# Optimization experiments

Hardware: AMD Instinct MI355X
Metric: run time of the kernel (lower is better)

## Reference

```python
import jax, jax.numpy as jnp
import numpy as np

N_NODES = 100000
N_EDGES = 1600000
D_IN = 128
D_HID = 128
N_CLS = 2


def gcn_conv(x, edge_index, W, b):
    """PyG GCNConv: add self-loops, symmetric normalization, linear, scatter-add, bias."""
    n = x.shape[0]
    loop = jnp.arange(n, dtype=edge_index.dtype)
    src = jnp.concatenate([edge_index[0], loop])  # [E+N]
    dst = jnp.concatenate([edge_index[1], loop])
    # degree computed on destination (col) after adding self-loops
    deg = jax.ops.segment_sum(jnp.ones_like(dst, dtype=x.dtype), dst, num_segments=n)
    dinv = jnp.where(deg > 0, jax.lax.rsqrt(deg), 0.0)
    norm = dinv[src] * dinv[dst]  # [E+N]
    h = x @ W  # [N, out]
    msg = h[src] * norm[:, None]  # [E+N, out]
    out = jax.ops.segment_sum(msg, dst, num_segments=n)
    return out + b


def setup_inputs() -> dict:
    key = jax.random.key(0)
    k1, k2, k3, k4 = jax.random.split(key, 4)
    x = jax.random.normal(k1, (N_NODES, D_IN), dtype=jnp.float32)
    edge_index = jax.random.randint(k2, (2, N_EDGES), 0, N_NODES, dtype=jnp.int64)
    W1 = jax.random.normal(k3, (D_IN, D_HID), dtype=jnp.float32) * (1.0 / np.sqrt(D_IN))
    b1 = jnp.zeros((D_HID,), dtype=jnp.float32)
    W2 = jax.random.normal(k4, (D_HID, N_CLS), dtype=jnp.float32) * (1.0 / np.sqrt(D_HID))
    b2 = jnp.zeros((N_CLS,), dtype=jnp.float32)
    return {"x": x, "edge_index": edge_index, "W1": W1, "b1": b1, "W2": W2, "b2": b2}


def reference(x, edge_index, W1, b1, W2, b2):
    h = gcn_conv(x, edge_index, W1, b1)
    h = jax.nn.relu(h)
    # training=False -> dropout skipped
    out = gcn_conv(h, edge_index, W2, b2)
    return out
```

## Files before the change

### kernel.cpp

```cpp
#include <hip/hip_runtime.h>
#include <hip/hip_fp16.h>
#include <cstdint>
#include <cstddef>

#define NN 100000
#define NE 1600000
#define D 128
#define NBK 782
#define NBLK_P 200
#define EPB 8000
#define CAP 3072

typedef _Float16 half8 __attribute__((ext_vector_type(8)));
typedef _Float16 half4v __attribute__((ext_vector_type(4)));
typedef float f32x4 __attribute__((ext_vector_type(4)));


__launch_bounds__(256)
__global__ void pscat_k(const int* __restrict__ ei, unsigned* __restrict__ gcnt,
                        unsigned* __restrict__ part,
                        const float* __restrict__ W, _Float16* __restrict__ Wt) {
    __shared__ unsigned hist[NBK];
    __shared__ unsigned run[NBK];
    int tid = threadIdx.x, b = blockIdx.x;
    for (int k = tid; k < NBK; k += 256) hist[k] = 0u;
    __syncthreads();
    int e0 = b * EPB;
    for (int i = tid * 4; i < EPB; i += 1024) {
        int4 d4 = *(const int4*)(ei + NE + e0 + i);
        atomicAdd(&hist[d4.x >> 7], 1u);
        atomicAdd(&hist[d4.y >> 7], 1u);
        atomicAdd(&hist[d4.z >> 7], 1u);
        atomicAdd(&hist[d4.w >> 7], 1u);
    }
    __syncthreads();
    for (int k = tid; k < NBK; k += 256) {
        unsigned c = hist[k];
        run[k] = c ? atomicAdd(&gcnt[k * 16], c) : 0u;
    }
    if (b < 64) {
        int idx = b * 256 + tid;
        int n = idx >> 7, kk = idx & 127;
        Wt[idx] = (_Float16)W[kk * 128 + n];
    }
    __syncthreads();
    for (int i = tid * 4; i < EPB; i += 1024) {
        int4 s4 = *(const int4*)(ei + e0 + i);
        int4 d4 = *(const int4*)(ei + NE + e0 + i);
        unsigned k, slot;
        k = (unsigned)(d4.x >> 7); slot = atomicAdd(&run[k], 1u);
        if (slot < CAP) part[(size_t)k * CAP + slot] = (unsigned)s4.x | ((unsigned)(d4.x & 127) << 20);
        k = (unsigned)(d4.y >> 7); slot = atomicAdd(&run[k], 1u);
        if (slot < CAP) part[(size_t)k * CAP + slot] = (unsigned)s4.y | ((unsigned)(d4.y & 127) << 20);
        k = (unsigned)(d4.z >> 7); slot = atomicAdd(&run[k], 1u);
        if (slot < CAP) part[(size_t)k * CAP + slot] = (unsigned)s4.z | ((unsigned)(d4.z & 127) << 20);
        k = (unsigned)(d4.w >> 7); slot = atomicAdd(&run[k], 1u);
        if (slot < CAP) part[(size_t)k * CAP + slot] = (unsigned)s4.w | ((unsigned)(d4.w & 127) << 20);
    }
}

__launch_bounds__(256)
__global__ void p4_csr_k(const unsigned* __restrict__ part, const unsigned* __restrict__ gcnt,
                         unsigned* __restrict__ rp, unsigned* __restrict__ re,
                         float* __restrict__ dinv, unsigned* __restrict__ col) {
    __shared__ unsigned c[128], p[128], run[128];
    int tid = threadIdx.x, k = blockIdx.x;
    int n0 = k << 7;
    int nodes = (NN - n0 < 128) ? (NN - n0) : 128;
    unsigned cnt = gcnt[k * 16];
    if (cnt > CAP) cnt = CAP;
    unsigned e0c = (unsigned)k * CAP;
    const unsigned* pk = part + (size_t)k * CAP;

    if (tid < 128) c[tid] = 0u;
    __syncthreads();
    for (unsigned t = tid; t < cnt; t += 256)
        atomicAdd(&c[(pk[t] >> 20) & 127], 1u);
    __syncthreads();

    unsigned myc = (tid < 128) ? c[tid] : 0u;
    if (tid < 128) p[tid] = myc;
    __syncthreads();
    for (int off = 1; off < 128; off <<= 1) {
        unsigned u = 0;
        if (tid < 128 && tid >= off) u = p[tid - off];
        __syncthreads();
        if (tid < 128) p[tid] += u;
        __syncthreads();
    }
    if (tid < 128) {
        unsigned excl = p[tid] - myc;
        run[tid] = excl;
        if (tid < nodes) {
            rp[n0 + tid] = e0c + excl;
            re[n0 + tid] = e0c + excl + myc;
            dinv[n0 + tid] = rsqrtf((float)(myc + 1u));
        }
    }
    __syncthreads();

    for (unsigned t = tid; t < cnt; t += 256) {
        unsigned v = pk[t];
        unsigned dlo = (v >> 20) & 127;
        unsigned pos = e0c + atomicAdd(&run[dlo], 1u);
        col[pos] = v & 0xFFFFFu;
    }
}

__launch_bounds__(256)
__global__ void gemm1_k(const float* __restrict__ x, const _Float16* __restrict__ Wt,
                        const float* __restrict__ dinv, _Float16* __restrict__ h) {
    __shared__ _Float16 wt[128 * 136];
    __shared__ _Float16 xs[128 * 72];
    int tid = threadIdx.x;
    int rb = blockIdx.x * 128;
    int w = tid >> 6, lane = tid & 63;
    int m = lane & 15, q4 = lane >> 4;

#pragma unroll
    for (int q = 0; q < 8; q++) {
        int idx = q * 256 + tid;
        int n = idx >> 4, k8 = (idx & 15) * 8;
        *(half8*)(&wt[n * 136 + k8]) = *(const half8*)(Wt + n * 128 + k8);
    }

    f32x4 acc[2][8];
#pragma unroll
    for (int rt = 0; rt < 2; rt++)
#pragma unroll
        for (int nt = 0; nt < 8; nt++) acc[rt][nt] = (f32x4){0.f, 0.f, 0.f, 0.f};

    for (int ks = 0; ks <= 64; ks += 64) {
        if (ks) __syncthreads();
#pragma unroll
        for (int q = 0; q < 8; q++) {
            int idx = q * 256 + tid;
            int row = idx >> 4;
            int c4 = (idx & 15) * 4;
            int gr = rb + row;
            float4 v = (gr < NN) ? *(const float4*)(x + (size_t)gr * 128 + ks + c4)
                                 : make_float4(0, 0, 0, 0);
            half4v hv = { (_Float16)v.x, (_Float16)v.y, (_Float16)v.z, (_Float16)v.w };
            *(half4v*)(&xs[row * 72 + c4]) = hv;
        }
        __syncthreads();

#pragma unroll
        for (int kc = 0; kc < 2; kc++) {
            half8 a0 = *(const half8*)(&xs[(w * 32 + m) * 72 + kc * 32 + q4 * 8]);
            half8 a1 = *(const half8*)(&xs[(w * 32 + 16 + m) * 72 + kc * 32 + q4 * 8]);
#pragma unroll
            for (int nt = 0; nt < 8; nt++) {
                half8 bf = *(const half8*)(&wt[(nt * 16 + m) * 136 + ks + kc * 32 + q4 * 8]);
                acc[0][nt] = __builtin_amdgcn_mfma_f32_16x16x32_f16(a0, bf, acc[0][nt], 0, 0, 0);
                acc[1][nt] = __builtin_amdgcn_mfma_f32_16x16x32_f16(a1, bf, acc[1][nt], 0, 0, 0);
            }
        }
    }

    float dv[2][4];
#pragma unroll
    for (int rt = 0; rt < 2; rt++)
#pragma unroll
        for (int r = 0; r < 4; r++) {
            int ri = rb + w * 32 + rt * 16 + q4 * 4 + r;
            dv[rt][r] = (ri < NN) ? dinv[ri] : 0.f;
        }
    __syncthreads();
#pragma unroll
    for (int rt = 0; rt < 2; rt++)
#pragma unroll
        for (int nt = 0; nt < 8; nt++)
#pragma unroll
            for (int r = 0; r < 4; r++)
                wt[(w * 32 + rt * 16 + q4 * 4 + r) * 136 + nt * 16 + m] =
                    (_Float16)(acc[rt][nt][r] * dv[rt][r]);
    __syncthreads();
#pragma unroll
    for (int q = 0; q < 8; q++) {
        int idx = q * 256 + tid;
        int row = idx >> 4;
        int c8 = (idx & 15) * 8;
        int gr = rb + row;
        if (gr < NN)
            *(half8*)(h + (size_t)gr * 128 + c8) = *(const half8*)(&wt[row * 136 + c8]);
    }
}

__launch_bounds__(256)
__global__ void agg1_k(const _Float16* __restrict__ h, const unsigned* __restrict__ rp,
                       const unsigned* __restrict__ re, const unsigned* __restrict__ col,
                       const float* __restrict__ dinv, const float* __restrict__ b1,
                       const float* __restrict__ W2, float* __restrict__ z) {
    int i = (blockIdx.x * 256 + threadIdx.x) >> 6;
    int lane = threadIdx.x & 63;
    if (i >= NN) return;
    unsigned si = __builtin_amdgcn_readfirstlane((unsigned)i);

    const __half2* hb = (const __half2*)h;
    unsigned p0 = __builtin_amdgcn_readfirstlane(rp[si]);
    unsigned p1 = __builtin_amdgcn_readfirstlane(re[si]);
    int deg = (int)(p1 - p0);

    unsigned cv = col[p0 + (unsigned)lane];

    int degc = deg > 64 ? 64 : deg;
    int R = (degc + 15) >> 4;
    float2 sv = __half22float2(hb[(size_t)si * 64u + lane]);
    float f = (float)(1 + degc - 16 * R);
    float ax = f * sv.x, ay = f * sv.y;

#define ROUND16(r)                                                           \
    {                                                                        \
        float2 vv[16];                                                       \
        _Pragma("unroll")                                                    \
        for (int t = 0; t < 16; t++) {                                       \
            int k = (r) * 16 + t;                                            \
            unsigned s = (k < degc) ? __builtin_amdgcn_readlane(cv, k) : si; \
            vv[t] = __half22float2(hb[(size_t)s * 64u + lane]);              \
        }                                                                    \
        ax += ((vv[0].x + vv[1].x) + (vv[2].x + vv[3].x))                    \
            + ((vv[4].x + vv[5].x) + (vv[6].x + vv[7].x))                    \
            + ((vv[8].x + vv[9].x) + (vv[10].x + vv[11].x))                  \
            + ((vv[12].x + vv[13].x) + (vv[14].x + vv[15].x));               \
        ay += ((vv[0].y + vv[1].y) + (vv[2].y + vv[3].y))                    \
            + ((vv[4].y + vv[5].y) + (vv[6].y + vv[7].y))                    \
            + ((vv[8].y + vv[9].y) + (vv[10].y + vv[11].y))                  \
            + ((vv[12].y + vv[13].y) + (vv[14].y + vv[15].y));               \
    }

    if (degc > 0)  ROUND16(0)
    if (degc > 16) ROUND16(1)
    if (degc > 32) ROUND16(2)
    if (degc > 48) ROUND16(3)
#undef ROUND16

    for (unsigned e = p0 + 64; e < p1; ++e) {
        unsigned s_ = __builtin_amdgcn_readfirstlane(col[e]);
        float2 v = __half22float2(hb[(size_t)s_ * 64u + lane]);
        ax += v.x;
        ay += v.y;
    }

    float di = dinv[si];
    ax *= di;
    ay *= di;

    float2 bv = ((const float2*)b1)[lane];
    float h0 = fmaxf(ax + bv.x, 0.f);
    float h1 = fmaxf(ay + bv.y, 0.f);

    float4 w = ((const float4*)W2)[lane];
    float pz0 = fmaf(h0, w.x, h1 * w.z);
    float pz1 = fmaf(h0, w.y, h1 * w.w);
#pragma unroll
    for (int off = 32; off > 0; off >>= 1) {
        pz0 += __shfl_down(pz0, off);
        pz1 += __shfl_down(pz1, off);
    }
    if (lane == 0) {
        float2* zp = (float2*)(z + (size_t)si * 2);
        *zp = make_float2(pz0 * di, pz1 * di);
    }
}

__launch_bounds__(256)
__global__ void agg2_k(const float* __restrict__ z, const unsigned* __restrict__ rp,
                       const unsigned* __restrict__ re, const unsigned* __restrict__ col,
                       const float* __restrict__ dinv, const float* __restrict__ b2,
                       float* __restrict__ out) {
    int i = (blockIdx.x * 256 + threadIdx.x) >> 4;
    int sl = threadIdx.x & 15;
    if (i >= NN) return;

    unsigned p0 = rp[i], p1 = re[i];
    float a0 = 0.f, a1 = 0.f;
    for (unsigned e = p0 + sl; e < p1; e += 16) {
        unsigned s = col[e];
        float2 v = ((const float2*)z)[s];
        a0 += v.x;
        a1 += v.y;
    }
#pragma unroll
    for (int off = 8; off > 0; off >>= 1) {
        a0 += __shfl_down(a0, off, 16);
        a1 += __shfl_down(a1, off, 16);
    }
    if (sl == 0) {
        float di = dinv[i];
        float2 zi = ((const float2*)z)[i];
        out[(size_t)i * 2]     = (a0 + zi.x) * di + b2[0];
        out[(size_t)i * 2 + 1] = (a1 + zi.y) * di + b2[1];
    }
}

extern "C" void kernel_launch(void* const* d_in, const int* in_sizes, int n_in,
                              void* d_out, int out_size, void* d_ws, size_t ws_size,
                              hipStream_t stream) {
    const float* x  = (const float*)d_in[0];
    const int*   ei = (const int*)d_in[1];
    const float* W1 = (const float*)d_in[2];
    const float* b1 = (const float*)d_in[3];
    const float* W2 = (const float*)d_in[4];
    const float* b2 = (const float*)d_in[5];
    float* out = (float*)d_out;

    char* ws = (char*)d_ws;
    unsigned* part = (unsigned*)(ws);
    unsigned* gcnt = (unsigned*)(ws + 9609216);
    _Float16* h    = (_Float16*)(ws);
    float*    z    = (float*)(ws + 25600000);
    float*    dinv = (float*)(ws + 26400000);
    unsigned* rp   = (unsigned*)(ws + 26800000);
    unsigned* re   = (unsigned*)(ws + 27200000);
    unsigned* col  = (unsigned*)(ws + 27600000);
    _Float16* Wt   = (_Float16*)(ws + 37300000);

    hipMemsetAsync(gcnt, 0, 782 * 16 * sizeof(unsigned), stream);
    pscat_k<<<NBLK_P, 256, 0, stream>>>(ei, gcnt, part, W1, Wt);
    p4_csr_k<<<NBK, 256, 0, stream>>>(part, gcnt, rp, re, dinv, col);

    gemm1_k<<<(NN + 127) / 128, 256, 0, stream>>>(x, Wt, dinv, h);
    agg1_k<<<(NN * 64 + 255) / 256, 256, 0, stream>>>(h, rp, re, col, dinv, b1, W2, z);
    agg2_k<<<(NN * 16 + 255) / 256, 256, 0, stream>>>(z, rp, re, col, dinv, b2, out);
}
```

Measured before the change: 221.1 us.

## Fuse CSR build kernel with first-layer GEMM into one kernel

Merges the per-bucket CSR construction kernel and the X·W1 MFMA GEMM into a single kernel, since both use 128-node blocks. The degree-based dinv is kept in shared memory and reused for row scaling, so it is not reloaded from global memory, and one kernel launch is removed. The h buffer moves to a separate workspace region because it previously aliased the partition buffer that the fused kernel still reads. The cost is a larger per-block shared-memory footprint, and the GEMM can no longer overlap independently with the CSR work.

After: 219.6 us. About the same (-0.7%).

```diff
diff --git a/kernel.cpp b/kernel.cpp
--- a/kernel.cpp
+++ b/kernel.cpp
@@ -60,41 +60,60 @@
 }
 
 __launch_bounds__(256)
-__global__ void p4_csr_k(const unsigned* __restrict__ part, const unsigned* __restrict__ gcnt,
-                         unsigned* __restrict__ rp, unsigned* __restrict__ re,
-                         float* __restrict__ dinv, unsigned* __restrict__ col) {
-    __shared__ unsigned c[128], p[128], run[128];
+__global__ void p4g_k(const unsigned* __restrict__ part, const unsigned* __restrict__ gcnt,
+                      const float* __restrict__ x, const _Float16* __restrict__ Wt,
+                      unsigned* __restrict__ rp, unsigned* __restrict__ re,
+                      float* __restrict__ dinv, unsigned* __restrict__ col,
+                      _Float16* __restrict__ h) {
+    __shared__ __align__(16) _Float16 wt[128 * 136];
+    __shared__ __align__(16) _Float16 xs[128 * 72];
+    __shared__ float dinvs[128];
+    unsigned* cc  = (unsigned*)xs;
+    unsigned* pp  = cc + 128;
+    unsigned* run = pp + 128;
     int tid = threadIdx.x, k = blockIdx.x;
     int n0 = k << 7;
     int nodes = (NN - n0 < 128) ? (NN - n0) : 128;
+    int w = tid >> 6, lane = tid & 63;
+    int m = lane & 15, q4 = lane >> 4;
+
+#pragma unroll
+    for (int q = 0; q < 8; q++) {
+        int idx = q * 256 + tid;
+        int n = idx >> 4, k8 = (idx & 15) * 8;
+        *(half8*)(&wt[n * 136 + k8]) = *(const half8*)(Wt + n * 128 + k8);
+    }
+
     unsigned cnt = gcnt[k * 16];
     if (cnt > CAP) cnt = CAP;
     unsigned e0c = (unsigned)k * CAP;
     const unsigned* pk = part + (size_t)k * CAP;
 
-    if (tid < 128) c[tid] = 0u;
+    if (tid < 128) cc[tid] = 0u;
     __syncthreads();
     for (unsigned t = tid; t < cnt; t += 256)
-        atomicAdd(&c[(pk[t] >> 20) & 127], 1u);
-    __syncthreads();
-
-    unsigned myc = (tid < 128) ? c[tid] : 0u;
-    if (tid < 128) p[tid] = myc;
+        atomicAdd(&cc[(pk[t] >> 20) & 127], 1u);
+    __syncthreads();
+
+    unsigned myc = (tid < 128) ? cc[tid] : 0u;
+    if (tid < 128) pp[tid] = myc;
     __syncthreads();
     for (int off = 1; off < 128; off <<= 1) {
         unsigned u = 0;
-        if (tid < 128 && tid >= off) u = p[tid - off];
+        if (tid < 128 && tid >= off) u = pp[tid - off];
         __syncthreads();
-        if (tid < 128) p[tid] += u;
+        if (tid < 128) pp[tid] += u;
         __syncthreads();
     }
     if (tid < 128) {
-        unsigned excl = p[tid] - myc;
+        unsigned excl = pp[tid] - myc;
         run[tid] = excl;
+        float dv = rsqrtf((float)(myc + 1u));
+        dinvs[tid] = dv;
         if (tid < nodes) {
             rp[n0 + tid] = e0c + excl;
             re[n0 + tid] = e0c + excl + myc;
-            dinv[n0 + tid] = rsqrtf((float)(myc + 1u));
+            dinv[n0 + tid] = dv;
         }
     }
     __syncthreads();
@@ -105,24 +124,7 @@
         unsigned pos = e0c + atomicAdd(&run[dlo], 1u);
         col[pos] = v & 0xFFFFFu;
     }
-}
-
-__launch_bounds__(256)
-__global__ void gemm1_k(const float* __restrict__ x, const _Float16* __restrict__ Wt,
-                        const float* __restrict__ dinv, _Float16* __restrict__ h) {
-    __shared__ _Float16 wt[128 * 136];
-    __shared__ _Float16 xs[128 * 72];
-    int tid = threadIdx.x;
-    int rb = blockIdx.x * 128;
-    int w = tid >> 6, lane = tid & 63;
-    int m = lane & 15, q4 = lane >> 4;
-
-#pragma unroll
-    for (int q = 0; q < 8; q++) {
-        int idx = q * 256 + tid;
-        int n = idx >> 4, k8 = (idx & 15) * 8;
-        *(half8*)(&wt[n * 136 + k8]) = *(const half8*)(Wt + n * 128 + k8);
-    }
+    __syncthreads();
 
     f32x4 acc[2][8];
 #pragma unroll
@@ -137,7 +139,7 @@
             int idx = q * 256 + tid;
             int row = idx >> 4;
             int c4 = (idx & 15) * 4;
-            int gr = rb + row;
+            int gr = n0 + row;
             float4 v = (gr < NN) ? *(const float4*)(x + (size_t)gr * 128 + ks + c4)
                                  : make_float4(0, 0, 0, 0);
             half4v hv = { (_Float16)v.x, (_Float16)v.y, (_Float16)v.z, (_Float16)v.w };
@@ -162,10 +164,8 @@
 #pragma unroll
     for (int rt = 0; rt < 2; rt++)
 #pragma unroll
-        for (int r = 0; r < 4; r++) {
-            int ri = rb + w * 32 + rt * 16 + q4 * 4 + r;
-            dv[rt][r] = (ri < NN) ? dinv[ri] : 0.f;
-        }
+        for (int r = 0; r < 4; r++)
+            dv[rt][r] = dinvs[w * 32 + rt * 16 + q4 * 4 + r];
     __syncthreads();
 #pragma unroll
     for (int rt = 0; rt < 2; rt++)
@@ -181,7 +181,7 @@
         int idx = q * 256 + tid;
         int row = idx >> 4;
         int c8 = (idx & 15) * 8;
-        int gr = rb + row;
+        int gr = n0 + row;
         if (gr < NN)
             *(half8*)(h + (size_t)gr * 128 + c8) = *(const half8*)(&wt[row * 136 + c8]);
     }
@@ -308,19 +308,17 @@
     char* ws = (char*)d_ws;
     unsigned* part = (unsigned*)(ws);
     unsigned* gcnt = (unsigned*)(ws + 9609216);
-    _Float16* h    = (_Float16*)(ws);
     float*    z    = (float*)(ws + 25600000);
     float*    dinv = (float*)(ws + 26400000);
     unsigned* rp   = (unsigned*)(ws + 26800000);
     unsigned* re   = (unsigned*)(ws + 27200000);
     unsigned* col  = (unsigned*)(ws + 27600000);
     _Float16* Wt   = (_Float16*)(ws + 37300000);
+    _Float16* h    = (_Float16*)(ws + 40000000);
 
     hipMemsetAsync(gcnt, 0, 782 * 16 * sizeof(unsigned), stream);
     pscat_k<<<NBLK_P, 256, 0, stream>>>(ei, gcnt, part, W1, Wt);
-    p4_csr_k<<<NBK, 256, 0, stream>>>(part, gcnt, rp, re, dinv, col);
-
-    gemm1_k<<<(NN + 127) / 128, 256, 0, stream>>>(x, Wt, dinv, h);
+    p4g_k<<<NBK, 256, 0, stream>>>(part, gcnt, x, Wt, rp, re, dinv, col, h);
     agg1_k<<<(NN * 64 + 255) / 256, 256, 0, stream>>>(h, rp, re, col, dinv, b1, W2, z);
     agg2_k<<<(NN * 16 + 255) / 256, 256, 0, stream>>>(z, rp, re, col, dinv, b2, out);
 }
```
